# Kernel tuning notes

Measured on AMD Instinct MI355X. Metric: run time of the kernel, lower is better.

## Reference

```python
import jax, jax.numpy as jnp
import numpy as np

N = 2048  # number of graph nodes


def setup_inputs() -> dict:
    key = jax.random.key(0)
    k1, k2, k3, k4 = jax.random.split(key, 4)
    # dense non-negative adjacency / association matrix
    A = jax.random.uniform(k1, (N, N), dtype=jnp.float32)
    # GTConv weights: layer0.conv1, layer0.conv2, layer1.conv1 (each (2,1,1,1))
    w1a = jax.random.normal(k2, (2, 1, 1, 1), dtype=jnp.float32)
    w1b = jax.random.normal(k3, (2, 1, 1, 1), dtype=jnp.float32)
    w2a = jax.random.normal(k4, (2, 1, 1, 1), dtype=jnp.float32)
    return {"A": A, "w1a": w1a, "w1b": w1b, "w2a": w2a}


def _gtconv(A4, w):
    # A4: (1,1,n,n); w: (2,1,1,1). softmax over dim=1 (singleton -> ones),
    # broadcast-multiply -> (2,1,n,n), sum over dim 0 -> (1,n,n)
    sw = jax.nn.softmax(w, axis=1)
    return jnp.sum(A4 * sw, axis=0)


def _norm(H):
    # H: (n,n). H <- diag(deg)^-1 @ (H + I), expressed as a row-scale
    # (identical math to the diagonal mm in the original).
    n = H.shape[0]
    H = H + jnp.eye(n, dtype=H.dtype)
    deg = jnp.sum(H, axis=1)
    deg = jnp.where(deg <= 1e-10, jnp.ones_like(deg), deg)
    return H / deg[:, None]


def reference(A, w1a, w1b, w2a):
    A4 = A[None, None]  # (1,1,n,n) after the forward's unsqueeze + broadcast
    # layer 0 (first=True)
    a = _gtconv(A4, w1a)            # (1,n,n)
    b = _gtconv(A4, w1b)            # (1,n,n)
    H = jnp.matmul(a, b)            # (1,n,n)
    # layer 1 (first=False): normalization of H[0], then bmm with conv(A)
    H_ = _norm(H[0])[None]          # (1,n,n)
    a2 = _gtconv(A4, w2a)           # (1,n,n)
    H2 = jnp.matmul(H_, a2)         # (1,n,n)
    return H2
```

## Files before the change

kernel.cpp:

```cpp
#include <hip/hip_runtime.h>
#include <stdint.h>

#define N 2048
#define TILE 128
#define BK 32

typedef unsigned short u16;
typedef __bf16 bf16x8 __attribute__((ext_vector_type(8)));
typedef unsigned short ushortx8 __attribute__((ext_vector_type(8)));
typedef float floatx4 __attribute__((ext_vector_type(4)));

static __device__ __forceinline__ u16 f2bf(float f) {
  unsigned int u = __builtin_bit_cast(unsigned int, f);
  return (u16)((u + 0x7fffu + ((u >> 16) & 1u)) >> 16);
}
static __device__ __forceinline__ float bf2f(u16 h) {
  unsigned int u = ((unsigned int)h) << 16;
  return __builtin_bit_cast(float, u);
}

static __device__ __forceinline__ void cp16(u16* lds, const u16* g) {
  __builtin_amdgcn_global_load_lds((const __attribute__((address_space(1))) void*)g,
                                   (__attribute__((address_space(3))) void*)lds,
                                   16, 0, 0);
}

__global__ void cast_tr(const float* __restrict__ A, u16* __restrict__ Ab,
                        u16* __restrict__ Abt) {
  __shared__ float tile[32][33];
  const int tx = threadIdx.x, ty = threadIdx.y;
  const int c = blockIdx.x * 32 + tx;
#pragma unroll
  for (int i = 0; i < 4; i++) {
    const int r = blockIdx.y * 32 + ty + i * 8;
    const float v = A[r * N + c];
    Ab[r * N + c] = f2bf(v);
    tile[ty + i * 8][tx] = v;
  }
  __syncthreads();
  const int r2 = blockIdx.y * 32 + tx;
#pragma unroll
  for (int i = 0; i < 4; i++) {
    const int c2 = blockIdx.x * 32 + ty + i * 8;
    Abt[c2 * N + r2] = f2bf(tile[tx][ty + i * 8]);
  }
}

__device__ __forceinline__ void gemm_tile(const u16* __restrict__ L,
                                          const u16* __restrict__ Rt,
                                          floatx4 acc[4][4]) {
  __shared__ __align__(16) u16 As[TILE * BK];
  __shared__ __align__(16) u16 Bs[TILE * BK];

  const int t = threadIdx.x;
  const int row0 = blockIdx.y * TILE;
  const int col0 = blockIdx.x * TILE;

  const int crow = t >> 2;
  const int coff = (t & 3) * 8;
  const u16* gA0 = L + (size_t)(row0 + crow) * N + coff;
  const u16* gA1 = gA0 + (size_t)64 * N;
  const u16* gB0 = Rt + (size_t)(col0 + crow) * N + coff;
  const u16* gB1 = gB0 + (size_t)64 * N;
  u16* lA0 = As + t * 8;
  u16* lA1 = As + 2048 + t * 8;
  u16* lB0 = Bs + t * 8;
  u16* lB1 = Bs + 2048 + t * 8;

  const int lane = t & 63;
  const int w = t >> 6;
  const int wr = (w >> 1) * 64;
  const int wc = (w & 1) * 64;
  const int lr = lane & 15;
  const int q = lane >> 4;

#pragma unroll
  for (int i = 0; i < 4; i++)
#pragma unroll
    for (int j = 0; j < 4; j++) acc[i][j] = (floatx4){0.f, 0.f, 0.f, 0.f};

  for (int k0 = 0; k0 < N; k0 += BK) {
    cp16(lA0, gA0 + k0);
    cp16(lA1, gA1 + k0);
    cp16(lB0, gB0 + k0);
    cp16(lB1, gB1 + k0);
    __syncthreads();

    bf16x8 a[4], b[4];
#pragma unroll
    for (int mt = 0; mt < 4; mt++)
      a[mt] = __builtin_bit_cast(
          bf16x8, *(const ushortx8*)&As[(wr + mt * 16 + lr) * BK + q * 8]);
#pragma unroll
    for (int nt = 0; nt < 4; nt++)
      b[nt] = __builtin_bit_cast(
          bf16x8, *(const ushortx8*)&Bs[(wc + nt * 16 + lr) * BK + q * 8]);
#pragma unroll
    for (int mt = 0; mt < 4; mt++)
#pragma unroll
      for (int nt = 0; nt < 4; nt++)
        acc[mt][nt] = __builtin_amdgcn_mfma_f32_16x16x32_bf16(
            a[mt], b[nt], acc[mt][nt], 0, 0, 0);
    __syncthreads();
  }
}

__global__ __launch_bounds__(256, 2) void gemm_aa(const u16* __restrict__ Ab,
                                                  const u16* __restrict__ Abt,
                                                  u16* __restrict__ Mb) {
  floatx4 acc[4][4];
  gemm_tile(Ab, Abt, acc);
  const int t = threadIdx.x;
  const int lane = t & 63, w = t >> 6;
  const int wr = (w >> 1) * 64, wc = (w & 1) * 64;
  const int lr = lane & 15, q = lane >> 4;
  const int row0 = blockIdx.y * TILE, col0 = blockIdx.x * TILE;
#pragma unroll
  for (int mt = 0; mt < 4; mt++)
#pragma unroll
    for (int r = 0; r < 4; r++) {
      const int rr = row0 + wr + mt * 16 + q * 4 + r;
#pragma unroll
      for (int nt = 0; nt < 4; nt++) {
        const int cc = col0 + wc + nt * 16 + lr;
        Mb[(size_t)rr * N + cc] = f2bf(acc[mt][nt][r]);
      }
    }
}

__global__ void rowsum_k(const u16* __restrict__ Mb, float* __restrict__ rdeg) {
  const int row = blockIdx.x;
  const int t = threadIdx.x;
  const ushortx8 v = *((const ushortx8*)(Mb + (size_t)row * N) + t);
  float s = 0.f;
#pragma unroll
  for (int j = 0; j < 8; j++) s += bf2f(v[j]);
#pragma unroll
  for (int off = 32; off > 0; off >>= 1) s += __shfl_down(s, off, 64);
  __shared__ float ws[4];
  if ((t & 63) == 0) ws[t >> 6] = s;
  __syncthreads();
  if (t == 0) {
    float d = 4.f * (ws[0] + ws[1] + ws[2] + ws[3]) + 1.f;
    if (d <= 1e-10f) d = 1.f;
    rdeg[row] = 1.f / d;
  }
}

__global__ __launch_bounds__(256, 2) void gemm_ma(const u16* __restrict__ Mb,
                                                  const u16* __restrict__ Abt,
                                                  const float* __restrict__ A,
                                                  const float* __restrict__ rdeg,
                                                  float* __restrict__ out) {
  floatx4 acc[4][4];
  gemm_tile(Mb, Abt, acc);
  const int t = threadIdx.x;
  const int lane = t & 63, w = t >> 6;
  const int wr = (w >> 1) * 64, wc = (w & 1) * 64;
  const int lr = lane & 15, q = lane >> 4;
  const int row0 = blockIdx.y * TILE, col0 = blockIdx.x * TILE;
#pragma unroll
  for (int mt = 0; mt < 4; mt++)
#pragma unroll
    for (int r = 0; r < 4; r++) {
      const int rr = row0 + wr + mt * 16 + q * 4 + r;
      const float rd = rdeg[rr];
#pragma unroll
      for (int nt = 0; nt < 4; nt++) {
        const int cc = col0 + wc + nt * 16 + lr;
        out[(size_t)rr * N + cc] =
            (8.f * acc[mt][nt][r] + 2.f * A[(size_t)rr * N + cc]) * rd;
      }
    }
}

extern "C" void kernel_launch(void* const* d_in, const int* in_sizes, int n_in,
                              void* d_out, int out_size, void* d_ws, size_t ws_size,
                              hipStream_t stream) {
  const float* A = (const float*)d_in[0];
  float* out = (float*)d_out;
  char* ws = (char*)d_ws;
  u16* Ab = (u16*)(ws);
  u16* Abt = (u16*)(ws + (size_t)N * N * 2);
  u16* Mb = (u16*)(ws + (size_t)N * N * 4);
  float* rdeg = (float*)(ws + (size_t)N * N * 6);

  cast_tr<<<dim3(N / 32, N / 32), dim3(32, 8), 0, stream>>>(A, Ab, Abt);
  gemm_aa<<<dim3(N / TILE, N / TILE), 256, 0, stream>>>(Ab, Abt, Mb);
  rowsum_k<<<N, 256, 0, stream>>>(Mb, rdeg);
  gemm_ma<<<dim3(N / TILE, N / TILE), 256, 0, stream>>>(Mb, Abt, A, rdeg, out);
}
```

Before: 160.3 us.

## Split-K GEMM blocks with register-prefetch pipeline and fused row-degree reduction

Each 128x128 output tile is now computed by a 512-thread block split into two K-halves whose partial accumulators are combined through LDS. The K loop uses register prefetching three stages ahead, double-buffered padded LDS, and one barrier per step, in place of the synchronous global_load_lds loop. The row-degree sum is folded into the first GEMM epilogue through LDS and global atomics, which removes the separate rowsum kernel; degrees now come from fp32 accumulators rather than the rounded bf16 values. The goal is better latency hiding and more waves per CU on a grid of only 256 tiles, at the cost of a memset launch, atomics and the split-K combine overhead.

```diff
diff --git a/kernel.cpp b/kernel.cpp
--- a/kernel.cpp
+++ b/kernel.cpp
@@ -4,6 +4,11 @@
 #define N 2048
 #define TILE 128
 #define BK 32
+#define KHALF 1024
+#define KI (KHALF / BK)
+#define LDSW 40
+#define ABUF 5120
+#define NN ((size_t)N * (size_t)N)
 
 typedef unsigned short u16;
 typedef __bf16 bf16x8 __attribute__((ext_vector_type(8)));
@@ -13,16 +18,6 @@
 static __device__ __forceinline__ u16 f2bf(float f) {
   unsigned int u = __builtin_bit_cast(unsigned int, f);
   return (u16)((u + 0x7fffu + ((u >> 16) & 1u)) >> 16);
-}
-static __device__ __forceinline__ float bf2f(u16 h) {
-  unsigned int u = ((unsigned int)h) << 16;
-  return __builtin_bit_cast(float, u);
-}
-
-static __device__ __forceinline__ void cp16(u16* lds, const u16* g) {
-  __builtin_amdgcn_global_load_lds((const __attribute__((address_space(1))) void*)g,
-                                   (__attribute__((address_space(3))) void*)lds,
-                                   16, 0, 0);
 }
 
 __global__ void cast_tr(const float* __restrict__ A, u16* __restrict__ Ab,
@@ -46,125 +41,182 @@
   }
 }
 
-__device__ __forceinline__ void gemm_tile(const u16* __restrict__ L,
+__device__ __forceinline__ void gemm_core(u16* smem, const u16* __restrict__ L,
                                           const u16* __restrict__ Rt,
                                           floatx4 acc[4][4]) {
-  __shared__ __align__(16) u16 As[TILE * BK];
-  __shared__ __align__(16) u16 Bs[TILE * BK];
-
-  const int t = threadIdx.x;
+  const int t = threadIdx.x;
+  const int g = t >> 8;
+  const int tl = t & 255;
   const int row0 = blockIdx.y * TILE;
   const int col0 = blockIdx.x * TILE;
 
-  const int crow = t >> 2;
-  const int coff = (t & 3) * 8;
-  const u16* gA0 = L + (size_t)(row0 + crow) * N + coff;
-  const u16* gA1 = gA0 + (size_t)64 * N;
-  const u16* gB0 = Rt + (size_t)(col0 + crow) * N + coff;
-  const u16* gB1 = gB0 + (size_t)64 * N;
-  u16* lA0 = As + t * 8;
-  u16* lA1 = As + 2048 + t * 8;
-  u16* lB0 = Bs + t * 8;
-  u16* lB1 = Bs + 2048 + t * 8;
+  const int srow = tl >> 1;
+  const int sc = (tl & 1) * 16;
+  const u16* gA = L + (size_t)(row0 + srow) * N + g * KHALF + sc;
+  const u16* gB = Rt + (size_t)(col0 + srow) * N + g * KHALF + sc;
+  const int wbA = g * (2 * ABUF) + srow * LDSW + sc;
+  const int wbB = 20480 + wbA;
 
   const int lane = t & 63;
-  const int w = t >> 6;
-  const int wr = (w >> 1) * 64;
-  const int wc = (w & 1) * 64;
+  const int wg = (t >> 6) & 3;
+  const int wr = (wg >> 1) * 64;
+  const int wc = (wg & 1) * 64;
   const int lr = lane & 15;
   const int q = lane >> 4;
+  const int raA = g * (2 * ABUF) + (wr + lr) * LDSW + q * 8;
+  const int raB = 20480 + g * (2 * ABUF) + (wc + lr) * LDSW + q * 8;
 
 #pragma unroll
   for (int i = 0; i < 4; i++)
 #pragma unroll
     for (int j = 0; j < 4; j++) acc[i][j] = (floatx4){0.f, 0.f, 0.f, 0.f};
 
-  for (int k0 = 0; k0 < N; k0 += BK) {
-    cp16(lA0, gA0 + k0);
-    cp16(lA1, gA1 + k0);
-    cp16(lB0, gB0 + k0);
-    cp16(lB1, gB1 + k0);
-    __syncthreads();
-
-    bf16x8 a[4], b[4];
-#pragma unroll
-    for (int mt = 0; mt < 4; mt++)
-      a[mt] = __builtin_bit_cast(
-          bf16x8, *(const ushortx8*)&As[(wr + mt * 16 + lr) * BK + q * 8]);
-#pragma unroll
-    for (int nt = 0; nt < 4; nt++)
-      b[nt] = __builtin_bit_cast(
-          bf16x8, *(const ushortx8*)&Bs[(wc + nt * 16 + lr) * BK + q * 8]);
+  ushortx8 rA[4][2], rB[4][2];
+#pragma unroll
+  for (int s = 0; s < 3; s++) {
+    rA[s][0] = *(const ushortx8*)(gA + s * BK);
+    rA[s][1] = *(const ushortx8*)(gA + s * BK + 8);
+    rB[s][0] = *(const ushortx8*)(gB + s * BK);
+    rB[s][1] = *(const ushortx8*)(gB + s * BK + 8);
+  }
+  *(ushortx8*)(&smem[wbA]) = rA[0][0];
+  *(ushortx8*)(&smem[wbA + 8]) = rA[0][1];
+  *(ushortx8*)(&smem[wbB]) = rB[0][0];
+  *(ushortx8*)(&smem[wbB + 8]) = rB[0][1];
+
+#define GSTEP(i, s)                                                           \
+  {                                                                           \
+    __syncthreads();                                                          \
+    if ((i) + 3 < KI) {                                                       \
+      rA[((s) + 3) & 3][0] = *(const ushortx8*)(gA + ((i) + 3) * BK);         \
+      rA[((s) + 3) & 3][1] = *(const ushortx8*)(gA + ((i) + 3) * BK + 8);     \
+      rB[((s) + 3) & 3][0] = *(const ushortx8*)(gB + ((i) + 3) * BK);         \
+      rB[((s) + 3) & 3][1] = *(const ushortx8*)(gB + ((i) + 3) * BK + 8);     \
+    }                                                                         \
+    bf16x8 af[4], bq[4];                                                      \
+    _Pragma("unroll") for (int mt = 0; mt < 4; mt++) af[mt] =                 \
+        __builtin_bit_cast(bf16x8, *(const ushortx8*)&smem[                   \
+            raA + ((s) & 1) * ABUF + mt * 16 * LDSW]);                        \
+    _Pragma("unroll") for (int nt = 0; nt < 4; nt++) bq[nt] =                 \
+        __builtin_bit_cast(bf16x8, *(const ushortx8*)&smem[                   \
+            raB + ((s) & 1) * ABUF + nt * 16 * LDSW]);                        \
+    _Pragma("unroll") for (int mt = 0; mt < 4; mt++)                          \
+        _Pragma("unroll") for (int nt = 0; nt < 4; nt++) acc[mt][nt] =        \
+            __builtin_amdgcn_mfma_f32_16x16x32_bf16(af[mt], bq[nt],           \
+                                                    acc[mt][nt], 0, 0, 0);    \
+    if ((i) + 1 < KI) {                                                       \
+      const int nb = (((s) + 1) & 1) * ABUF;                                  \
+      *(ushortx8*)(&smem[wbA + nb]) = rA[((s) + 1) & 3][0];                   \
+      *(ushortx8*)(&smem[wbA + nb + 8]) = rA[((s) + 1) & 3][1];               \
+      *(ushortx8*)(&smem[wbB + nb]) = rB[((s) + 1) & 3][0];                   \
+      *(ushortx8*)(&smem[wbB + nb + 8]) = rB[((s) + 1) & 3][1];               \
+    }                                                                         \
+  }
+
+  for (int io = 0; io < KI; io += 4) {
+    GSTEP(io + 0, 0)
+    GSTEP(io + 1, 1)
+    GSTEP(io + 2, 2)
+    GSTEP(io + 3, 3)
+  }
+#undef GSTEP
+}
+
+__device__ __forceinline__ void combine(u16* smem, floatx4 acc[4][4]) {
+  float* smf = (float*)smem;
+  const int t = threadIdx.x;
+  const int g = t >> 8;
+  const int lane = t & 63;
+  const int wg = (t >> 6) & 3;
+  __syncthreads();
+  if (g == 1) {
 #pragma unroll
     for (int mt = 0; mt < 4; mt++)
 #pragma unroll
       for (int nt = 0; nt < 4; nt++)
-        acc[mt][nt] = __builtin_amdgcn_mfma_f32_16x16x32_bf16(
-            a[mt], b[nt], acc[mt][nt], 0, 0, 0);
-    __syncthreads();
-  }
-}
-
-__global__ __launch_bounds__(256, 2) void gemm_aa(const u16* __restrict__ Ab,
-                                                  const u16* __restrict__ Abt,
-                                                  u16* __restrict__ Mb) {
+        *(floatx4*)&smf[wg * 4096 + (mt * 4 + nt) * 256 + lane * 4] =
+            acc[mt][nt];
+  }
+  __syncthreads();
+  if (g == 0) {
+#pragma unroll
+    for (int mt = 0; mt < 4; mt++)
+#pragma unroll
+      for (int nt = 0; nt < 4; nt++)
+        acc[mt][nt] += *(const floatx4*)&smf[wg * 4096 + (mt * 4 + nt) * 256 +
+                                             lane * 4];
+  }
+}
+
+__global__ __launch_bounds__(512, 2) void gemm1(const u16* __restrict__ Ab,
+                                                const u16* __restrict__ Abt,
+                                                u16* __restrict__ Mb,
+                                                float* __restrict__ deg) {
+  __shared__ __align__(16) u16 smem[40960];
   floatx4 acc[4][4];
-  gemm_tile(Ab, Abt, acc);
-  const int t = threadIdx.x;
-  const int lane = t & 63, w = t >> 6;
-  const int wr = (w >> 1) * 64, wc = (w & 1) * 64;
+  gemm_core(smem, Ab, Abt, acc);
+  combine(smem, acc);
+
+  float* rs = (float*)smem + 16384;
+  const int t = threadIdx.x;
+  const int row0 = blockIdx.y * TILE, col0 = blockIdx.x * TILE;
+  if (t < TILE) rs[t] = 0.f;
+  __syncthreads();
+  if ((t >> 8) == 0) {
+    const int lane = t & 63, wg = (t >> 6) & 3;
+    const int wr = (wg >> 1) * 64, wc = (wg & 1) * 64;
+    const int lr = lane & 15, q = lane >> 4;
+    float trs[4][4];
+#pragma unroll
+    for (int mt = 0; mt < 4; mt++)
+#pragma unroll
+      for (int r = 0; r < 4; r++) trs[mt][r] = 0.f;
+#pragma unroll
+    for (int mt = 0; mt < 4; mt++)
+#pragma unroll
+      for (int nt = 0; nt < 4; nt++)
+#pragma unroll
+        for (int r = 0; r < 4; r++) {
+          const float v = acc[mt][nt][r];
+          const int rr = row0 + wr + mt * 16 + q * 4 + r;
+          const int cc = col0 + wc + nt * 16 + lr;
+          Mb[(size_t)rr * N + cc] = f2bf(v);
+          trs[mt][r] += v;
+        }
+#pragma unroll
+    for (int mt = 0; mt < 4; mt++)
+#pragma unroll
+      for (int r = 0; r < 4; r++)
+        atomicAdd(&rs[wr + mt * 16 + q * 4 + r], trs[mt][r]);
+  }
+  __syncthreads();
+  if (t < TILE) atomicAdd(&deg[row0 + t], rs[t]);
+}
+
+__global__ __launch_bounds__(512, 2) void gemm2(const u16* __restrict__ Mb,
+                                                const u16* __restrict__ Abt,
+                                                const float* __restrict__ A,
+                                                const float* __restrict__ deg,
+                                                float* __restrict__ out) {
+  __shared__ __align__(16) u16 smem[40960];
+  floatx4 acc[4][4];
+  gemm_core(smem, Mb, Abt, acc);
+  combine(smem, acc);
+
+  const int t = threadIdx.x;
+  if ((t >> 8) != 0) return;
+  const int row0 = blockIdx.y * TILE, col0 = blockIdx.x * TILE;
+  const int lane = t & 63, wg = (t >> 6) & 3;
+  const int wr = (wg >> 1) * 64, wc = (wg & 1) * 64;
   const int lr = lane & 15, q = lane >> 4;
-  const int row0 = blockIdx.y * TILE, col0 = blockIdx.x * TILE;
 #pragma unroll
   for (int mt = 0; mt < 4; mt++)
 #pragma unroll
     for (int r = 0; r < 4; r++) {
       const int rr = row0 + wr + mt * 16 + q * 4 + r;
-#pragma unroll
-      for (int nt = 0; nt < 4; nt++) {
-        const int cc = col0 + wc + nt * 16 + lr;
-        Mb[(size_t)rr * N + cc] = f2bf(acc[mt][nt][r]);
-      }
-    }
-}
-
-__global__ void rowsum_k(const u16* __restrict__ Mb, float* __restrict__ rdeg) {
-  const int row = blockIdx.x;
-  const int t = threadIdx.x;
-  const ushortx8 v = *((const ushortx8*)(Mb + (size_t)row * N) + t);
-  float s = 0.f;
-#pragma unroll
-  for (int j = 0; j < 8; j++) s += bf2f(v[j]);
-#pragma unroll
-  for (int off = 32; off > 0; off >>= 1) s += __shfl_down(s, off, 64);
-  __shared__ float ws[4];
-  if ((t & 63) == 0) ws[t >> 6] = s;
-  __syncthreads();
-  if (t == 0) {
-    float d = 4.f * (ws[0] + ws[1] + ws[2] + ws[3]) + 1.f;
-    if (d <= 1e-10f) d = 1.f;
-    rdeg[row] = 1.f / d;
-  }
-}
-
-__global__ __launch_bounds__(256, 2) void gemm_ma(const u16* __restrict__ Mb,
-                                                  const u16* __restrict__ Abt,
-                                                  const float* __restrict__ A,
-                                                  const float* __restrict__ rdeg,
-                                                  float* __restrict__ out) {
-  floatx4 acc[4][4];
-  gemm_tile(Mb, Abt, acc);
-  const int t = threadIdx.x;
-  const int lane = t & 63, w = t >> 6;
-  const int wr = (w >> 1) * 64, wc = (w & 1) * 64;
-  const int lr = lane & 15, q = lane >> 4;
-  const int row0 = blockIdx.y * TILE, col0 = blockIdx.x * TILE;
-#pragma unroll
-  for (int mt = 0; mt < 4; mt++)
-#pragma unroll
-    for (int r = 0; r < 4; r++) {
-      const int rr = row0 + wr + mt * 16 + q * 4 + r;
-      const float rd = rdeg[rr];
+      float d = 4.f * deg[rr] + 1.f;
+      if (d <= 1e-10f) d = 1.f;
+      const float rd = 1.f / d;
 #pragma unroll
       for (int nt = 0; nt < 4; nt++) {
         const int cc = col0 + wc + nt * 16 + lr;
@@ -180,13 +232,13 @@
   const float* A = (const float*)d_in[0];
   float* out = (float*)d_out;
   char* ws = (char*)d_ws;
-  u16* Ab = (u16*)(ws);
-  u16* Abt = (u16*)(ws + (size_t)N * N * 2);
-  u16* Mb = (u16*)(ws + (size_t)N * N * 4);
-  float* rdeg = (float*)(ws + (size_t)N * N * 6);
-
+  u16* Ab = (u16*)ws;
+  u16* Abt = (u16*)(ws + NN * 2);
+  u16* Mb = (u16*)(ws + NN * 4);
+  float* deg = (float*)(ws + NN * 6);
+
+  hipMemsetAsync(deg, 0, N * sizeof(float), stream);
   cast_tr<<<dim3(N / 32, N / 32), dim3(32, 8), 0, stream>>>(A, Ab, Abt);
-  gemm_aa<<<dim3(N / TILE, N / TILE), 256, 0, stream>>>(Ab, Abt, Mb);
-  rowsum_k<<<N, 256, 0, stream>>>(Mb, rdeg);
-  gemm_ma<<<dim3(N / TILE, N / TILE), 256, 0, stream>>>(Mb, Abt, A, rdeg, out);
-}
+  gemm1<<<dim3(16, 16), 512, 0, stream>>>(Ab, Abt, Mb, deg);
+  gemm2<<<dim3(16, 16), 512, 0, stream>>>(Mb, Abt, A, deg, out);
+}
```

After: 142.9 us. -10.9%, faster.
